# Performance work log

Hardware: AMD Instinct MI355X
Metric: run time of the kernel (lower is better)

## Reference

```python
import jax, jax.numpy as jnp
import numpy as np
from jax import lax

B, L, F = 32, 2048, 76   # batch, seq_len, feat_dim
H = 128                  # conv hidden channels
D = 128                  # prototype dim (last 1x1 conv)
P = 128                  # number of prototypes
CLASS_SIZE = 2


def setup_inputs() -> dict:
    key = jax.random.key(0)
    ks = jax.random.split(key, 8)
    w = lambda k, shape: jax.random.normal(k, shape, jnp.float32) * 0.05
    return {
        "x": jax.random.normal(ks[0], (B, L, F), jnp.float32),
        "W1": w(ks[1], (H, F, 5)), "b1": jnp.zeros((H,), jnp.float32),
        "W2": w(ks[2], (H, H, 5)), "b2": jnp.zeros((H,), jnp.float32),
        "W3": w(ks[3], (H, H, 5)), "b3": jnp.zeros((H,), jnp.float32),
        "Wo1": w(ks[4], (D, H)), "bo1": jnp.zeros((D,), jnp.float32),
        "Wo2": w(ks[5], (D, D)), "bo2": jnp.zeros((D,), jnp.float32),
        "prototypes": jax.random.uniform(ks[6], (P, D), jnp.float32),
        "protop_classes": jnp.concatenate([jnp.zeros(P // 2, jnp.int32), jnp.ones(P // 2, jnp.int32)]),
    }


def _conv1d_same(h, W, b):
    # h: (B, C, L), W: (O, C, K=5), symmetric padding 2 == torch padding=k//2
    y = lax.conv_general_dilated(h, W, window_strides=(1,), padding=[(2, 2)],
                                 dimension_numbers=("NCW", "OIW", "NCW"))
    return y + b[None, :, None]


def _maxpool2(h):
    return lax.reduce_window(h, -jnp.inf, lax.max, (1, 1, 2), (1, 1, 2), "VALID")


def reference(x, W1, b1, W2, b2, W3, b3, Wo1, bo1, Wo2, bo2, prototypes, protop_classes):
    h = jnp.transpose(x, (0, 2, 1))  # (B, F, L)
    for W, b in ((W1, b1), (W2, b2), (W3, b3)):
        h = _maxpool2(jax.nn.relu(_conv1d_same(h, W, b)))
    # 1x1 convs as channel matmuls
    h = jax.nn.relu(jnp.einsum("bcl,oc->bol", h, Wo1) + bo1[None, :, None])
    h = jax.nn.relu(jnp.einsum("bcl,oc->bol", h, Wo2) + bo2[None, :, None])
    f = jnp.transpose(h, (0, 2, 1))  # (B, Lp=256, D)
    # l2_conv via ||a-b||^2 = ||a||^2 - 2 a.b + ||b||^2 (same math, GEMM form)
    d2 = (jnp.sum(f * f, axis=-1, keepdims=True)
          - 2.0 * jnp.einsum("bld,pd->blp", f, prototypes)
          + jnp.sum(prototypes * prototypes, axis=-1))  # (B, Lp, P)
    dis = jnp.sqrt(jnp.maximum(d2, 1e-12))
    min_dis = jnp.min(dis, axis=1)  # (B, P): min over patches
    # dis2sim, 'log' activation
    sim = jnp.log((min_dis + 1.0) / (min_dis + 1e-4))
    # init_weights: last_layer.weight[i,j] = 1 if protop_classes[j]==i else -0.5
    lw = jnp.where(protop_classes[None, :] == jnp.arange(CLASS_SIZE)[:, None], 1.0, -0.5)
    out = jax.nn.sigmoid(sim @ lw.T)  # (B, CLASS_SIZE)
    return out, min_dis
```

## Files before the change

### kernel.cpp

```cpp
#include <hip/hip_runtime.h>
#include <cmath>


typedef __attribute__((ext_vector_type(8))) short short8;
typedef __attribute__((ext_vector_type(4))) float f32x4;

__device__ __forceinline__ unsigned short f2bf(float v) {
    union { float f; unsigned u; } x; x.f = v;
    unsigned r = x.u + 0x7fffu + ((x.u >> 16) & 1u);
    return (unsigned short)(r >> 16);
}
__device__ __forceinline__ float bf2f(unsigned short b) {
    union { unsigned u; float f; } x; x.u = ((unsigned)b) << 16;
    return x.f;
}

__global__ __launch_bounds__(256)
void convert_x_kernel(const float* __restrict__ x, unsigned short* __restrict__ xb)
{
    int t = blockIdx.x * 256 + threadIdx.x;
    int row = t / 12, c0 = (t % 12) * 8;
    unsigned short v[8];
#pragma unroll
    for (int j = 0; j < 8; ++j) {
        int c = c0 + j;
        v[j] = (c < 76) ? f2bf(x[(size_t)row * 76 + c]) : (unsigned short)0;
    }
    *(uint4*)&xb[(size_t)row * 96 + c0] = *(uint4*)v;
}

__device__ void pack_conv_w(int t, int total, const float* __restrict__ W, int C,
                            unsigned short* __restrict__ dst)
{
    if (t >= total) return;
    int lane = t & 63, rest = t >> 6;
    int mf = rest & 7; rest >>= 3;
    int kk = rest % 5, cc = rest / 5;
    int m = mf * 16 + (lane & 15);
    int cb = cc * 32 + (lane >> 4) * 8;
    unsigned short v[8];
#pragma unroll
    for (int j = 0; j < 8; ++j) {
        int c = cb + j;
        v[j] = (c < C) ? f2bf(W[((size_t)m * C + c) * 5 + kk]) : (unsigned short)0;
    }
    *(uint4*)&dst[(size_t)t * 8] = *(uint4*)v;
}

__device__ void pack_mat(int t, const float* __restrict__ M, unsigned short* __restrict__ dst)
{
    if (t >= 2048) return;
    int lane = t & 63, mf = (t >> 6) & 7, cc = t >> 9;
    int m = mf * 16 + (lane & 15);
    int c0 = cc * 32 + (lane >> 4) * 8;
    unsigned short v[8];
#pragma unroll
    for (int j = 0; j < 8; ++j) v[j] = f2bf(M[(size_t)m * 128 + c0 + j]);
    *(uint4*)&dst[(size_t)t * 8] = *(uint4*)v;
}

__global__ __launch_bounds__(256)
void prep_weights_kernel(const float* __restrict__ W1, const float* __restrict__ W2,
                         const float* __restrict__ W3, const float* __restrict__ Wo1,
                         const float* __restrict__ Wo2, const float* __restrict__ protos,
                         unsigned short* A1, unsigned short* A2, unsigned short* A3,
                         unsigned short* AW1, unsigned short* AW2, unsigned short* AP,
                         float* pn)
{
    int t = blockIdx.x * 256 + threadIdx.x;
    switch (blockIdx.y) {
    case 0: pack_conv_w(t, 7680,  W1, 76,  A1); break;
    case 1: pack_conv_w(t, 10240, W2, 128, A2); break;
    case 2: pack_conv_w(t, 10240, W3, 128, A3); break;
    case 3: pack_mat(t, Wo1, AW1); break;
    case 4: pack_mat(t, Wo2, AW2); break;
    case 5: pack_mat(t, protos, AP); break;
    case 6:
        if (t < 128) {
            float s = 0.f;
            for (int d = 0; d < 128; ++d) {
                float v = bf2f(f2bf(protos[(size_t)t * 128 + d]));
                s = fmaf(v, v, s);
            }
            pn[t] = s;
        }
        break;
    }
}

template <int CPAD_G, int LIN>
__global__ __launch_bounds__(256)
void conv_mfma(const unsigned short* __restrict__ in, const unsigned short* __restrict__ Af,
               const float* __restrict__ bias, unsigned short* __restrict__ out)
{
    constexpr int NCH    = CPAD_G / 32;
    constexpr int CPAD_L = CPAD_G + 8;
    constexpr int LOUT   = LIN / 2;
    constexpr int CW     = CPAD_G / 8;

    __shared__ __align__(16) unsigned short s_in[68 * CPAD_L];
    __shared__ float s_bias[128];

    const int tid = threadIdx.x;
    const int b   = blockIdx.y;
    const int l0  = blockIdx.x * 64;

    if (tid < 128) s_bias[tid] = bias[tid];

    for (int idx = tid; idx < 68 * CW; idx += 256) {
        int pos = idx / CW, co = (idx % CW) * 8;
        int l = l0 - 2 + pos;
        uint4 v = make_uint4(0u, 0u, 0u, 0u);
        if (l >= 0 && l < LIN)
            v = *(const uint4*)&in[((size_t)b * LIN + l) * CPAD_G + co];
        *(uint4*)&s_in[pos * CPAD_L + co] = v;
    }
    __syncthreads();

    const int lane = tid & 63;
    const int wid  = tid >> 6;
    const int mh   = (wid & 1) * 4;
    const int nh   = (wid >> 1) * 32;
    const int lc   = lane & 15;
    const int lk   = (lane >> 4) * 8;

    const f32x4 zero = {0.f, 0.f, 0.f, 0.f};
    f32x4 acc[4][2];
#pragma unroll
    for (int i = 0; i < 4; ++i)
#pragma unroll
        for (int j = 0; j < 2; ++j) acc[i][j] = zero;

    for (int cc = 0; cc < NCH; ++cc) {
#pragma unroll
        for (int kk = 0; kk < 5; ++kk) {
            const int step = cc * 5 + kk;
            short8 a[4];
#pragma unroll
            for (int i = 0; i < 4; ++i)
                a[i] = *(const short8*)&Af[(((size_t)step * 8 + mh + i) * 64 + lane) * 8];
            short8 bb[2];
#pragma unroll
            for (int j = 0; j < 2; ++j) {
                int row = nh + j * 16 + lc + kk;
                bb[j] = *(const short8*)&s_in[row * CPAD_L + cc * 32 + lk];
            }
#pragma unroll
            for (int i = 0; i < 4; ++i)
#pragma unroll
                for (int j = 0; j < 2; ++j)
                    acc[i][j] = __builtin_amdgcn_mfma_f32_16x16x32_bf16(a[i], bb[j], acc[i][j], 0, 0, 0);
        }
    }

    const int lp0 = l0 >> 1;
#pragma unroll
    for (int i = 0; i < 4; ++i) {
        const int ch0 = (mh + i) * 16 + (lane >> 4) * 4;
#pragma unroll
        for (int j = 0; j < 2; ++j) {
            const int n = nh + j * 16 + lc;
            unsigned short pk[4];
#pragma unroll
            for (int r = 0; r < 4; ++r) {
                float v = fmaxf(acc[i][j][r] + s_bias[ch0 + r], 0.f);
                float o = __shfl_xor(v, 1);
                pk[r] = f2bf(fmaxf(v, o));
            }
            if ((lc & 1) == 0)
                *(uint2*)&out[((size_t)b * LOUT + lp0 + (n >> 1)) * 128 + ch0] = *(uint2*)pk;
        }
    }
}

__global__ __launch_bounds__(256)
void head_mfma(const unsigned short* __restrict__ f,
               const unsigned short* __restrict__ AW1, const float* __restrict__ bo1,
               const unsigned short* __restrict__ AW2, const float* __restrict__ bo2,
               const unsigned short* __restrict__ AP,  const float* __restrict__ pn,
               float* __restrict__ partmin)
{
    constexpr int CP = 136;
    __shared__ __align__(16) unsigned short s_f[64 * CP];
    __shared__ float s_fn[64];
    __shared__ float s_part[4 * 64];
    __shared__ float s_min[2 * 128];

    const int tid = threadIdx.x;
    const int b   = blockIdx.y;
    const int p0  = blockIdx.x * 64;

    for (int idx = tid; idx < 64 * 16; idx += 256) {
        int pos = idx >> 4, co = (idx & 15) * 8;
        *(uint4*)&s_f[pos * CP + co] =
            *(const uint4*)&f[((size_t)b * 256 + p0 + pos) * 128 + co];
    }
    __syncthreads();

    const int lane = tid & 63;
    const int wid  = tid >> 6;
    const int mh   = (wid & 1) * 4;
    const int nh   = (wid >> 1) * 32;
    const int lc   = lane & 15;
    const int lk   = (lane >> 4) * 8;

    const f32x4 zero = {0.f, 0.f, 0.f, 0.f};
    f32x4 acc[4][2];

    auto gemm = [&](const unsigned short* __restrict__ A) {
#pragma unroll
        for (int i = 0; i < 4; ++i)
#pragma unroll
            for (int j = 0; j < 2; ++j) acc[i][j] = zero;
        for (int cc = 0; cc < 4; ++cc) {
            short8 a[4];
#pragma unroll
            for (int i = 0; i < 4; ++i)
                a[i] = *(const short8*)&A[(((size_t)cc * 8 + mh + i) * 64 + lane) * 8];
            short8 bb[2];
#pragma unroll
            for (int j = 0; j < 2; ++j)
                bb[j] = *(const short8*)&s_f[(nh + j * 16 + lc) * CP + cc * 32 + lk];
#pragma unroll
            for (int i = 0; i < 4; ++i)
#pragma unroll
                for (int j = 0; j < 2; ++j)
                    acc[i][j] = __builtin_amdgcn_mfma_f32_16x16x32_bf16(a[i], bb[j], acc[i][j], 0, 0, 0);
        }
    };

    auto store_relu = [&](const float* __restrict__ bias) {
        __syncthreads();
#pragma unroll
        for (int i = 0; i < 4; ++i) {
            const int ch0 = (mh + i) * 16 + (lane >> 4) * 4;
#pragma unroll
            for (int j = 0; j < 2; ++j) {
                const int n = nh + j * 16 + lc;
                unsigned short pk[4];
#pragma unroll
                for (int r = 0; r < 4; ++r)
                    pk[r] = f2bf(fmaxf(acc[i][j][r] + bias[ch0 + r], 0.f));
                *(uint2*)&s_f[n * CP + ch0] = *(uint2*)pk;
            }
        }
        __syncthreads();
    };

    gemm(AW1); store_relu(bo1);
    gemm(AW2); store_relu(bo2);

    {
        int n = tid >> 2, part = tid & 3;
        float s = 0.f;
        for (int c = part * 32; c < part * 32 + 32; ++c) {
            float v = bf2f(s_f[n * CP + c]);
            s = fmaf(v, v, s);
        }
        s_part[part * 64 + n] = s;
    }
    __syncthreads();
    if (tid < 64)
        s_fn[tid] = s_part[tid] + s_part[64 + tid] + s_part[128 + tid] + s_part[192 + tid];
    __syncthreads();

    gemm(AP);

#pragma unroll
    for (int i = 0; i < 4; ++i) {
#pragma unroll
        for (int r = 0; r < 4; ++r) {
            const int p = (mh + i) * 16 + (lane >> 4) * 4 + r;
            float m = 3.0e38f;
#pragma unroll
            for (int j = 0; j < 2; ++j) {
                const int n = nh + j * 16 + lc;
                float d2 = s_fn[n] + pn[p] - 2.f * acc[i][j][r];
                m = fminf(m, sqrtf(fmaxf(d2, 1e-12f)));
            }
#pragma unroll
            for (int s = 1; s < 16; s <<= 1)
                m = fminf(m, __shfl_xor(m, s));
            if (lc == 0) s_min[(wid >> 1) * 128 + p] = m;
        }
    }
    __syncthreads();
    if (tid < 128)
        partmin[((size_t)b * 4 + blockIdx.x) * 128 + tid] = fminf(s_min[tid], s_min[128 + tid]);
}

__global__ __launch_bounds__(128)
void finalize_kernel(const float* __restrict__ partmin,
                     const int* __restrict__ classes,
                     float* __restrict__ out)
{
    __shared__ float r0[128], r1[128];
    const int b = blockIdx.x, p = threadIdx.x;
    float m = partmin[((size_t)b * 4) * 128 + p];
#pragma unroll
    for (int q = 1; q < 4; ++q)
        m = fminf(m, partmin[((size_t)b * 4 + q) * 128 + p]);
    out[64 + b * 128 + p] = m;

    float sim = logf((m + 1.0f) / (m + 1e-4f));
    int cls = classes[p];
    r0[p] = (cls == 0) ? sim : -0.5f * sim;
    r1[p] = (cls == 1) ? sim : -0.5f * sim;
    __syncthreads();
    for (int s = 64; s > 0; s >>= 1) {
        if (p < s) { r0[p] += r0[p + s]; r1[p] += r1[p + s]; }
        __syncthreads();
    }
    if (p == 0) {
        out[b * 2 + 0] = 1.f / (1.f + expf(-r0[0]));
        out[b * 2 + 1] = 1.f / (1.f + expf(-r1[0]));
    }
}

extern "C" void kernel_launch(void* const* d_in, const int* in_sizes, int n_in,
                              void* d_out, int out_size, void* d_ws, size_t ws_size,
                              hipStream_t stream)
{
    (void)in_sizes; (void)n_in; (void)out_size; (void)ws_size;
    const float* x    = (const float*)d_in[0];
    const float* W1   = (const float*)d_in[1];
    const float* b1   = (const float*)d_in[2];
    const float* W2   = (const float*)d_in[3];
    const float* b2   = (const float*)d_in[4];
    const float* W3   = (const float*)d_in[5];
    const float* b3   = (const float*)d_in[6];
    const float* Wo1  = (const float*)d_in[7];
    const float* bo1  = (const float*)d_in[8];
    const float* Wo2  = (const float*)d_in[9];
    const float* bo2  = (const float*)d_in[10];
    const float* prot = (const float*)d_in[11];
    const int*   cls  = (const int*)d_in[12];
    float* out = (float*)d_out;

    char* ws = (char*)d_ws;
    unsigned short* xb = (unsigned short*)(ws);
    unsigned short* h1 = (unsigned short*)(ws + 12582912);
    unsigned short* h2 = (unsigned short*)(ws);
    unsigned short* h3 = (unsigned short*)(ws + 4194304);
    const size_t FR = 20971520;
    unsigned short* A1  = (unsigned short*)(ws + FR);
    unsigned short* A2  = (unsigned short*)(ws + FR + 122880);
    unsigned short* A3  = (unsigned short*)(ws + FR + 286720);
    unsigned short* AW1 = (unsigned short*)(ws + FR + 450560);
    unsigned short* AW2 = (unsigned short*)(ws + FR + 483328);
    unsigned short* AP  = (unsigned short*)(ws + FR + 516096);
    float*          pn  = (float*)(ws + FR + 548864);
    float*          pm  = (float*)(ws + FR + 549376);

    convert_x_kernel<<<3072, 256, 0, stream>>>(x, xb);
    prep_weights_kernel<<<dim3(40, 7), 256, 0, stream>>>(W1, W2, W3, Wo1, Wo2, prot,
                                                         A1, A2, A3, AW1, AW2, AP, pn);
    conv_mfma< 96, 2048><<<dim3(32, 32), 256, 0, stream>>>(xb, A1, b1, h1);
    conv_mfma<128, 1024><<<dim3(16, 32), 256, 0, stream>>>(h1, A2, b2, h2);
    conv_mfma<128,  512><<<dim3( 8, 32), 256, 0, stream>>>(h2, A3, b3, h3);
    head_mfma<<<dim3(4, 32), 256, 0, stream>>>(h3, AW1, bo1, AW2, bo2, AP, pn, pm);
    finalize_kernel<<<32, 128, 0, stream>>>(pm, cls, out);
}
```

Baseline: 155.0 us.

## Fuse input conversion into conv1 and conv3 with head, use atomicMin reduction

Drops the separate fp32-to-bf16 conversion kernel by having conv1 read fp32 x directly and convert while filling shared memory. Fuses conv3 with the 1x1 head and prototype distance so h3 never goes to global memory, and replaces the partial-min buffer with atomicMin on float bits, initialised in the prep kernel. It also changes the warp tiling to 2 M-fragments by 4 N-fragments per wave. This saves two launches and a few global round trips, at the cost of a smaller 32-row head tile per block and atomic traffic.

```diff
diff --git a/kernel.cpp b/kernel.cpp
--- a/kernel.cpp
+++ b/kernel.cpp
@@ -13,20 +13,6 @@
 __device__ __forceinline__ float bf2f(unsigned short b) {
     union { unsigned u; float f; } x; x.u = ((unsigned)b) << 16;
     return x.f;
-}
-
-__global__ __launch_bounds__(256)
-void convert_x_kernel(const float* __restrict__ x, unsigned short* __restrict__ xb)
-{
-    int t = blockIdx.x * 256 + threadIdx.x;
-    int row = t / 12, c0 = (t % 12) * 8;
-    unsigned short v[8];
-#pragma unroll
-    for (int j = 0; j < 8; ++j) {
-        int c = c0 + j;
-        v[j] = (c < 76) ? f2bf(x[(size_t)row * 76 + c]) : (unsigned short)0;
-    }
-    *(uint4*)&xb[(size_t)row * 96 + c0] = *(uint4*)v;
 }
 
 __device__ void pack_conv_w(int t, int total, const float* __restrict__ W, int C,
@@ -65,7 +51,7 @@
                          const float* __restrict__ Wo2, const float* __restrict__ protos,
                          unsigned short* A1, unsigned short* A2, unsigned short* A3,
                          unsigned short* AW1, unsigned short* AW2, unsigned short* AP,
-                         float* pn)
+                         float* pn, unsigned* pm_bits)
 {
     int t = blockIdx.x * 256 + threadIdx.x;
     switch (blockIdx.y) {
@@ -85,20 +71,18 @@
             pn[t] = s;
         }
         break;
-    }
-}
-
-template <int CPAD_G, int LIN>
+    case 7:
+        if (t < 4096) pm_bits[t] = 0x7F800000u;
+        break;
+    }
+}
+
 __global__ __launch_bounds__(256)
-void conv_mfma(const unsigned short* __restrict__ in, const unsigned short* __restrict__ Af,
-               const float* __restrict__ bias, unsigned short* __restrict__ out)
-{
-    constexpr int NCH    = CPAD_G / 32;
-    constexpr int CPAD_L = CPAD_G + 8;
-    constexpr int LOUT   = LIN / 2;
-    constexpr int CW     = CPAD_G / 8;
-
-    __shared__ __align__(16) unsigned short s_in[68 * CPAD_L];
+void conv1_mfma(const float* __restrict__ x, const unsigned short* __restrict__ Af,
+                const float* __restrict__ bias, unsigned short* __restrict__ out)
+{
+    constexpr int LIN = 2048, LOUT = 1024, CPL = 104;
+    __shared__ __align__(16) unsigned short s_in[68 * CPL];
     __shared__ float s_bias[128];
 
     const int tid = threadIdx.x;
@@ -107,59 +91,57 @@
 
     if (tid < 128) s_bias[tid] = bias[tid];
 
-    for (int idx = tid; idx < 68 * CW; idx += 256) {
-        int pos = idx / CW, co = (idx % CW) * 8;
+    for (int idx = tid; idx < 68 * 24; idx += 256) {
+        int pos = idx / 24, c0 = (idx % 24) * 4;
         int l = l0 - 2 + pos;
-        uint4 v = make_uint4(0u, 0u, 0u, 0u);
-        if (l >= 0 && l < LIN)
-            v = *(const uint4*)&in[((size_t)b * LIN + l) * CPAD_G + co];
-        *(uint4*)&s_in[pos * CPAD_L + co] = v;
+        unsigned short v[4] = {0, 0, 0, 0};
+        if (c0 < 76 && l >= 0 && l < LIN) {
+            float4 xv = *(const float4*)&x[((size_t)b * LIN + l) * 76 + c0];
+            v[0] = f2bf(xv.x); v[1] = f2bf(xv.y); v[2] = f2bf(xv.z); v[3] = f2bf(xv.w);
+        }
+        *(uint2*)&s_in[pos * CPL + c0] = *(uint2*)v;
     }
     __syncthreads();
 
     const int lane = tid & 63;
-    const int wid  = tid >> 6;
-    const int mh   = (wid & 1) * 4;
-    const int nh   = (wid >> 1) * 32;
+    const int mf0  = (tid >> 6) * 2;
     const int lc   = lane & 15;
     const int lk   = (lane >> 4) * 8;
 
     const f32x4 zero = {0.f, 0.f, 0.f, 0.f};
-    f32x4 acc[4][2];
-#pragma unroll
-    for (int i = 0; i < 4; ++i)
-#pragma unroll
-        for (int j = 0; j < 2; ++j) acc[i][j] = zero;
-
-    for (int cc = 0; cc < NCH; ++cc) {
+    f32x4 acc[2][4];
+#pragma unroll
+    for (int i = 0; i < 2; ++i)
+#pragma unroll
+        for (int j = 0; j < 4; ++j) acc[i][j] = zero;
+
+    for (int cc = 0; cc < 3; ++cc) {
 #pragma unroll
         for (int kk = 0; kk < 5; ++kk) {
             const int step = cc * 5 + kk;
-            short8 a[4];
-#pragma unroll
-            for (int i = 0; i < 4; ++i)
-                a[i] = *(const short8*)&Af[(((size_t)step * 8 + mh + i) * 64 + lane) * 8];
-            short8 bb[2];
-#pragma unroll
-            for (int j = 0; j < 2; ++j) {
-                int row = nh + j * 16 + lc + kk;
-                bb[j] = *(const short8*)&s_in[row * CPAD_L + cc * 32 + lk];
-            }
-#pragma unroll
-            for (int i = 0; i < 4; ++i)
-#pragma unroll
-                for (int j = 0; j < 2; ++j)
+            short8 a[2];
+#pragma unroll
+            for (int i = 0; i < 2; ++i)
+                a[i] = *(const short8*)&Af[(((size_t)step * 8 + mf0 + i) * 64 + lane) * 8];
+            short8 bb[4];
+#pragma unroll
+            for (int j = 0; j < 4; ++j)
+                bb[j] = *(const short8*)&s_in[(j * 16 + lc + kk) * CPL + cc * 32 + lk];
+#pragma unroll
+            for (int i = 0; i < 2; ++i)
+#pragma unroll
+                for (int j = 0; j < 4; ++j)
                     acc[i][j] = __builtin_amdgcn_mfma_f32_16x16x32_bf16(a[i], bb[j], acc[i][j], 0, 0, 0);
         }
     }
 
     const int lp0 = l0 >> 1;
 #pragma unroll
-    for (int i = 0; i < 4; ++i) {
-        const int ch0 = (mh + i) * 16 + (lane >> 4) * 4;
-#pragma unroll
-        for (int j = 0; j < 2; ++j) {
-            const int n = nh + j * 16 + lc;
+    for (int i = 0; i < 2; ++i) {
+        const int ch0 = (mf0 + i) * 16 + (lane >> 4) * 4;
+#pragma unroll
+        for (int j = 0; j < 4; ++j) {
+            const int n = j * 16 + lc;
             unsigned short pk[4];
 #pragma unroll
             for (int r = 0; r < 4; ++r) {
@@ -174,132 +156,254 @@
 }
 
 __global__ __launch_bounds__(256)
-void head_mfma(const unsigned short* __restrict__ f,
-               const unsigned short* __restrict__ AW1, const float* __restrict__ bo1,
-               const unsigned short* __restrict__ AW2, const float* __restrict__ bo2,
-               const unsigned short* __restrict__ AP,  const float* __restrict__ pn,
-               float* __restrict__ partmin)
-{
-    constexpr int CP = 136;
-    __shared__ __align__(16) unsigned short s_f[64 * CP];
-    __shared__ float s_fn[64];
-    __shared__ float s_part[4 * 64];
-    __shared__ float s_min[2 * 128];
+void conv2_mfma(const unsigned short* __restrict__ in, const unsigned short* __restrict__ Af,
+                const float* __restrict__ bias, unsigned short* __restrict__ out)
+{
+    constexpr int LIN = 1024, LOUT = 512, CPL = 136;
+    __shared__ __align__(16) unsigned short s_in[68 * CPL];
+    __shared__ float s_bias[128];
 
     const int tid = threadIdx.x;
     const int b   = blockIdx.y;
-    const int p0  = blockIdx.x * 64;
-
-    for (int idx = tid; idx < 64 * 16; idx += 256) {
+    const int l0  = blockIdx.x * 64;
+
+    if (tid < 128) s_bias[tid] = bias[tid];
+
+    for (int idx = tid; idx < 68 * 16; idx += 256) {
         int pos = idx >> 4, co = (idx & 15) * 8;
-        *(uint4*)&s_f[pos * CP + co] =
-            *(const uint4*)&f[((size_t)b * 256 + p0 + pos) * 128 + co];
+        int l = l0 - 2 + pos;
+        uint4 v = make_uint4(0u, 0u, 0u, 0u);
+        if (l >= 0 && l < LIN)
+            v = *(const uint4*)&in[((size_t)b * LIN + l) * 128 + co];
+        *(uint4*)&s_in[pos * CPL + co] = v;
     }
     __syncthreads();
 
     const int lane = tid & 63;
-    const int wid  = tid >> 6;
-    const int mh   = (wid & 1) * 4;
-    const int nh   = (wid >> 1) * 32;
+    const int mf0  = (tid >> 6) * 2;
     const int lc   = lane & 15;
     const int lk   = (lane >> 4) * 8;
 
     const f32x4 zero = {0.f, 0.f, 0.f, 0.f};
-    f32x4 acc[4][2];
-
-    auto gemm = [&](const unsigned short* __restrict__ A) {
-#pragma unroll
-        for (int i = 0; i < 4; ++i)
-#pragma unroll
-            for (int j = 0; j < 2; ++j) acc[i][j] = zero;
+    f32x4 acc[2][4];
+#pragma unroll
+    for (int i = 0; i < 2; ++i)
+#pragma unroll
+        for (int j = 0; j < 4; ++j) acc[i][j] = zero;
+
+    for (int cc = 0; cc < 4; ++cc) {
+#pragma unroll
+        for (int kk = 0; kk < 5; ++kk) {
+            const int step = cc * 5 + kk;
+            short8 a[2];
+#pragma unroll
+            for (int i = 0; i < 2; ++i)
+                a[i] = *(const short8*)&Af[(((size_t)step * 8 + mf0 + i) * 64 + lane) * 8];
+            short8 bb[4];
+#pragma unroll
+            for (int j = 0; j < 4; ++j)
+                bb[j] = *(const short8*)&s_in[(j * 16 + lc + kk) * CPL + cc * 32 + lk];
+#pragma unroll
+            for (int i = 0; i < 2; ++i)
+#pragma unroll
+                for (int j = 0; j < 4; ++j)
+                    acc[i][j] = __builtin_amdgcn_mfma_f32_16x16x32_bf16(a[i], bb[j], acc[i][j], 0, 0, 0);
+        }
+    }
+
+    const int lp0 = l0 >> 1;
+#pragma unroll
+    for (int i = 0; i < 2; ++i) {
+        const int ch0 = (mf0 + i) * 16 + (lane >> 4) * 4;
+#pragma unroll
+        for (int j = 0; j < 4; ++j) {
+            const int n = j * 16 + lc;
+            unsigned short pk[4];
+#pragma unroll
+            for (int r = 0; r < 4; ++r) {
+                float v = fmaxf(acc[i][j][r] + s_bias[ch0 + r], 0.f);
+                float o = __shfl_xor(v, 1);
+                pk[r] = f2bf(fmaxf(v, o));
+            }
+            if ((lc & 1) == 0)
+                *(uint2*)&out[((size_t)b * LOUT + lp0 + (n >> 1)) * 128 + ch0] = *(uint2*)pk;
+        }
+    }
+}
+
+__global__ __launch_bounds__(256)
+void conv3_head(const unsigned short* __restrict__ in, const unsigned short* __restrict__ Af,
+                const float* __restrict__ bias,
+                const unsigned short* __restrict__ AW1, const float* __restrict__ bo1,
+                const unsigned short* __restrict__ AW2, const float* __restrict__ bo2,
+                const unsigned short* __restrict__ AP,  const float* __restrict__ pn,
+                unsigned* __restrict__ pm_bits)
+{
+    constexpr int LIN = 512, CPL = 136, CP = 136;
+    __shared__ __align__(16) unsigned short s_in[68 * CPL];
+    __shared__ __align__(16) unsigned short s_f[32 * CP];
+    __shared__ float s_bias[128];
+    __shared__ float s_part[4 * 32];
+    __shared__ float s_fn[32];
+
+    const int tid = threadIdx.x;
+    const int b   = blockIdx.y;
+    const int l0  = blockIdx.x * 64;
+
+    if (tid < 128) s_bias[tid] = bias[tid];
+
+    for (int idx = tid; idx < 68 * 16; idx += 256) {
+        int pos = idx >> 4, co = (idx & 15) * 8;
+        int l = l0 - 2 + pos;
+        uint4 v = make_uint4(0u, 0u, 0u, 0u);
+        if (l >= 0 && l < LIN)
+            v = *(const uint4*)&in[((size_t)b * LIN + l) * 128 + co];
+        *(uint4*)&s_in[pos * CPL + co] = v;
+    }
+    __syncthreads();
+
+    const int lane = tid & 63;
+    const int mf0  = (tid >> 6) * 2;
+    const int lc   = lane & 15;
+    const int lk   = (lane >> 4) * 8;
+
+    const f32x4 zero = {0.f, 0.f, 0.f, 0.f};
+
+    f32x4 acc[2][4];
+#pragma unroll
+    for (int i = 0; i < 2; ++i)
+#pragma unroll
+        for (int j = 0; j < 4; ++j) acc[i][j] = zero;
+
+    for (int cc = 0; cc < 4; ++cc) {
+#pragma unroll
+        for (int kk = 0; kk < 5; ++kk) {
+            const int step = cc * 5 + kk;
+            short8 a[2];
+#pragma unroll
+            for (int i = 0; i < 2; ++i)
+                a[i] = *(const short8*)&Af[(((size_t)step * 8 + mf0 + i) * 64 + lane) * 8];
+            short8 bb[4];
+#pragma unroll
+            for (int j = 0; j < 4; ++j)
+                bb[j] = *(const short8*)&s_in[(j * 16 + lc + kk) * CPL + cc * 32 + lk];
+#pragma unroll
+            for (int i = 0; i < 2; ++i)
+#pragma unroll
+                for (int j = 0; j < 4; ++j)
+                    acc[i][j] = __builtin_amdgcn_mfma_f32_16x16x32_bf16(a[i], bb[j], acc[i][j], 0, 0, 0);
+        }
+    }
+
+#pragma unroll
+    for (int i = 0; i < 2; ++i) {
+        const int ch0 = (mf0 + i) * 16 + (lane >> 4) * 4;
+#pragma unroll
+        for (int j = 0; j < 4; ++j) {
+            const int n = j * 16 + lc;
+            unsigned short pk[4];
+#pragma unroll
+            for (int r = 0; r < 4; ++r) {
+                float v = fmaxf(acc[i][j][r] + s_bias[ch0 + r], 0.f);
+                float o = __shfl_xor(v, 1);
+                pk[r] = f2bf(fmaxf(v, o));
+            }
+            if ((lc & 1) == 0)
+                *(uint2*)&s_f[(n >> 1) * CP + ch0] = *(uint2*)pk;
+        }
+    }
+    __syncthreads();
+
+    f32x4 hacc[2][2];
+
+    auto gemm32 = [&](const unsigned short* __restrict__ A) {
+#pragma unroll
+        for (int i = 0; i < 2; ++i)
+#pragma unroll
+            for (int j = 0; j < 2; ++j) hacc[i][j] = zero;
         for (int cc = 0; cc < 4; ++cc) {
-            short8 a[4];
-#pragma unroll
-            for (int i = 0; i < 4; ++i)
-                a[i] = *(const short8*)&A[(((size_t)cc * 8 + mh + i) * 64 + lane) * 8];
+            short8 a[2];
+#pragma unroll
+            for (int i = 0; i < 2; ++i)
+                a[i] = *(const short8*)&A[(((size_t)cc * 8 + mf0 + i) * 64 + lane) * 8];
             short8 bb[2];
 #pragma unroll
             for (int j = 0; j < 2; ++j)
-                bb[j] = *(const short8*)&s_f[(nh + j * 16 + lc) * CP + cc * 32 + lk];
-#pragma unroll
-            for (int i = 0; i < 4; ++i)
+                bb[j] = *(const short8*)&s_f[(j * 16 + lc) * CP + cc * 32 + lk];
+#pragma unroll
+            for (int i = 0; i < 2; ++i)
 #pragma unroll
                 for (int j = 0; j < 2; ++j)
-                    acc[i][j] = __builtin_amdgcn_mfma_f32_16x16x32_bf16(a[i], bb[j], acc[i][j], 0, 0, 0);
+                    hacc[i][j] = __builtin_amdgcn_mfma_f32_16x16x32_bf16(a[i], bb[j], hacc[i][j], 0, 0, 0);
         }
     };
 
-    auto store_relu = [&](const float* __restrict__ bias) {
+    auto store_relu32 = [&](const float* __restrict__ bv) {
         __syncthreads();
 #pragma unroll
-        for (int i = 0; i < 4; ++i) {
-            const int ch0 = (mh + i) * 16 + (lane >> 4) * 4;
+        for (int i = 0; i < 2; ++i) {
+            const int ch0 = (mf0 + i) * 16 + (lane >> 4) * 4;
 #pragma unroll
             for (int j = 0; j < 2; ++j) {
-                const int n = nh + j * 16 + lc;
+                const int n = j * 16 + lc;
                 unsigned short pk[4];
 #pragma unroll
                 for (int r = 0; r < 4; ++r)
-                    pk[r] = f2bf(fmaxf(acc[i][j][r] + bias[ch0 + r], 0.f));
+                    pk[r] = f2bf(fmaxf(hacc[i][j][r] + bv[ch0 + r], 0.f));
                 *(uint2*)&s_f[n * CP + ch0] = *(uint2*)pk;
             }
         }
         __syncthreads();
     };
 
-    gemm(AW1); store_relu(bo1);
-    gemm(AW2); store_relu(bo2);
-
-    {
+    gemm32(AW1); store_relu32(bo1);
+    gemm32(AW2); store_relu32(bo2);
+
+    if (tid < 128) {
         int n = tid >> 2, part = tid & 3;
         float s = 0.f;
         for (int c = part * 32; c < part * 32 + 32; ++c) {
             float v = bf2f(s_f[n * CP + c]);
             s = fmaf(v, v, s);
         }
-        s_part[part * 64 + n] = s;
-    }
-    __syncthreads();
-    if (tid < 64)
-        s_fn[tid] = s_part[tid] + s_part[64 + tid] + s_part[128 + tid] + s_part[192 + tid];
-    __syncthreads();
-
-    gemm(AP);
-
-#pragma unroll
-    for (int i = 0; i < 4; ++i) {
+        s_part[part * 32 + n] = s;
+    }
+    __syncthreads();
+    if (tid < 32)
+        s_fn[tid] = s_part[tid] + s_part[32 + tid] + s_part[64 + tid] + s_part[96 + tid];
+    __syncthreads();
+
+    gemm32(AP);
+
+#pragma unroll
+    for (int i = 0; i < 2; ++i) {
 #pragma unroll
         for (int r = 0; r < 4; ++r) {
-            const int p = (mh + i) * 16 + (lane >> 4) * 4 + r;
+            const int p = (mf0 + i) * 16 + (lane >> 4) * 4 + r;
             float m = 3.0e38f;
 #pragma unroll
             for (int j = 0; j < 2; ++j) {
-                const int n = nh + j * 16 + lc;
-                float d2 = s_fn[n] + pn[p] - 2.f * acc[i][j][r];
+                const int n = j * 16 + lc;
+                float d2 = s_fn[n] + pn[p] - 2.f * hacc[i][j][r];
                 m = fminf(m, sqrtf(fmaxf(d2, 1e-12f)));
             }
 #pragma unroll
             for (int s = 1; s < 16; s <<= 1)
                 m = fminf(m, __shfl_xor(m, s));
-            if (lc == 0) s_min[(wid >> 1) * 128 + p] = m;
-        }
-    }
-    __syncthreads();
-    if (tid < 128)
-        partmin[((size_t)b * 4 + blockIdx.x) * 128 + tid] = fminf(s_min[tid], s_min[128 + tid]);
+            if (lc == 0)
+                atomicMin(&pm_bits[(size_t)b * 128 + p], __float_as_uint(m));
+        }
+    }
 }
 
 __global__ __launch_bounds__(128)
-void finalize_kernel(const float* __restrict__ partmin,
+void finalize_kernel(const float* __restrict__ pm,
                      const int* __restrict__ classes,
                      float* __restrict__ out)
 {
     __shared__ float r0[128], r1[128];
     const int b = blockIdx.x, p = threadIdx.x;
-    float m = partmin[((size_t)b * 4) * 128 + p];
-#pragma unroll
-    for (int q = 1; q < 4; ++q)
-        m = fminf(m, partmin[((size_t)b * 4 + q) * 128 + p]);
+    float m = pm[(size_t)b * 128 + p];
     out[64 + b * 128 + p] = m;
 
     float sim = logf((m + 1.0f) / (m + 1e-4f));
@@ -338,11 +442,9 @@
     float* out = (float*)d_out;
 
     char* ws = (char*)d_ws;
-    unsigned short* xb = (unsigned short*)(ws);
-    unsigned short* h1 = (unsigned short*)(ws + 12582912);
-    unsigned short* h2 = (unsigned short*)(ws);
-    unsigned short* h3 = (unsigned short*)(ws + 4194304);
-    const size_t FR = 20971520;
+    unsigned short* h1 = (unsigned short*)(ws);
+    unsigned short* h2 = (unsigned short*)(ws + 8388608);
+    const size_t FR = 12582912;
     unsigned short* A1  = (unsigned short*)(ws + FR);
     unsigned short* A2  = (unsigned short*)(ws + FR + 122880);
     unsigned short* A3  = (unsigned short*)(ws + FR + 286720);
@@ -350,14 +452,12 @@
     unsigned short* AW2 = (unsigned short*)(ws + FR + 483328);
     unsigned short* AP  = (unsigned short*)(ws + FR + 516096);
     float*          pn  = (float*)(ws + FR + 548864);
-    float*          pm  = (float*)(ws + FR + 549376);
-
-    convert_x_kernel<<<3072, 256, 0, stream>>>(x, xb);
-    prep_weights_kernel<<<dim3(40, 7), 256, 0, stream>>>(W1, W2, W3, Wo1, Wo2, prot,
-                                                         A1, A2, A3, AW1, AW2, AP, pn);
-    conv_mfma< 96, 2048><<<dim3(32, 32), 256, 0, stream>>>(xb, A1, b1, h1);
-    conv_mfma<128, 1024><<<dim3(16, 32), 256, 0, stream>>>(h1, A2, b2, h2);
-    conv_mfma<128,  512><<<dim3( 8, 32), 256, 0, stream>>>(h2, A3, b3, h3);
-    head_mfma<<<dim3(4, 32), 256, 0, stream>>>(h3, AW1, bo1, AW2, bo2, AP, pn, pm);
-    finalize_kernel<<<32, 128, 0, stream>>>(pm, cls, out);
-}
+    unsigned*       pm  = (unsigned*)(ws + FR + 549376);
+
+    prep_weights_kernel<<<dim3(40, 8), 256, 0, stream>>>(W1, W2, W3, Wo1, Wo2, prot,
+                                                         A1, A2, A3, AW1, AW2, AP, pn, pm);
+    conv1_mfma<<<dim3(32, 32), 256, 0, stream>>>(x,  A1, b1, h1);
+    conv2_mfma<<<dim3(16, 32), 256, 0, stream>>>(h1, A2, b2, h2);
+    conv3_head<<<dim3(8, 32), 256, 0, stream>>>(h2, A3, b3, AW1, bo1, AW2, bo2, AP, pn, pm);
+    finalize_kernel<<<32, 128, 0, stream>>>((const float*)pm, cls, out);
+}
```

New measurement: 133.1 us. 14.1% less time.
